# Performance work log

Hardware: AMD Instinct MI355X
Metric: run time of the kernel (lower is better)

Reference implementation:

```python
import jax, jax.numpy as jnp
import numpy as np

B, C, H, W = 8, 256, 64, 64
CM = C // 4          # mask channels (theta/phi out) = 64
CI = C - CM          # img channels = 192
EPS = 1e-5


def setup_inputs() -> dict:
    key = jax.random.key(0)
    ks = jax.random.split(key, 12)
    return {
        "x": jax.random.normal(ks[0], (B, C, H, W), dtype=jnp.float32),
        "g_w": jax.random.normal(ks[1], (C, C), dtype=jnp.float32) * 0.05,
        "g_b": jax.random.normal(ks[2], (C,), dtype=jnp.float32) * 0.01,
        "theta_w": jax.random.normal(ks[3], (CM, CM), dtype=jnp.float32) * 0.1,
        "theta_b": jax.random.normal(ks[4], (CM,), dtype=jnp.float32) * 0.01,
        "phi_w": jax.random.normal(ks[5], (CM, CI), dtype=jnp.float32) * 0.06,
        "phi_b": jax.random.normal(ks[6], (CM,), dtype=jnp.float32) * 0.01,
        "W_w": jax.random.normal(ks[7], (C, C), dtype=jnp.float32) * 0.05,
        "W_b": jax.random.normal(ks[8], (C,), dtype=jnp.float32) * 0.01,
        "bn_gamma": jax.random.normal(ks[9], (C,), dtype=jnp.float32) * 0.1 + 1.0,
        "bn_beta": jax.random.normal(ks[10], (C,), dtype=jnp.float32) * 0.01,
        "bn_mean": jax.random.normal(ks[11], (C,), dtype=jnp.float32) * 0.1,
        "bn_var": jnp.ones((C,), dtype=jnp.float32),
    }


def _conv1x1(t, w, b):
    # [B,Cin,H,W] x [Cout,Cin] -> [B,Cout,H,W]
    return jnp.einsum('bchw,oc->bohw', t, w) + b[None, :, None, None]


def _maxpool2(t):
    b, c, h, w = t.shape
    return t.reshape(b, c, h // 2, 2, w // 2, 2).max(axis=(3, 5))


def reference(x, g_w, g_b, theta_w, theta_b, phi_w, phi_b, W_w, W_b,
              bn_gamma, bn_beta, bn_mean, bn_var):
    b, c, h, w = x.shape
    ci = c // 4
    mask_ch = x[:, :ci]          # [B, C/4, H, W]
    img_ch = x[:, ci:]           # [B, 3C/4, H, W]

    # g: conv1x1 then 2x2 maxpool -> [B, C, N'] -> [B, N', C]
    g_x = _maxpool2(_conv1x1(x, g_w, g_b)).reshape(b, c, -1).transpose(0, 2, 1)
    # theta: conv1x1 on mask -> [B, N, C/4]
    theta_x = _conv1x1(mask_ch, theta_w, theta_b).reshape(b, ci, -1).transpose(0, 2, 1)
    # phi: conv1x1 on img then pool -> [B, C/4, N']
    phi_x = _maxpool2(_conv1x1(img_ch, phi_w, phi_b)).reshape(b, ci, -1)

    f = jnp.einsum('bnc,bcm->bnm', theta_x, phi_x)     # [B, N, N']
    f_div_C = jax.nn.softmax(f, axis=-1)
    y = jnp.einsum('bnm,bmc->bnc', f_div_C, g_x)       # [B, N, C]
    y = y.transpose(0, 2, 1).reshape(b, c, h, w)

    W_y = _conv1x1(y, W_w, W_b)
    # BatchNorm (inference form with running stats)
    inv = jax.lax.rsqrt(bn_var + EPS)
    W_y = (W_y - bn_mean[None, :, None, None]) * (inv * bn_gamma)[None, :, None, None] \
          + bn_beta[None, :, None, None]
    return W_y + x
```

## Files before the change

### kernel.cpp

```cpp
#include <hip/hip_runtime.h>
#include <hip/hip_bf16.h>

typedef __hip_bfloat16 bf16;
typedef unsigned short ushort;
typedef unsigned int uint;
typedef __attribute__((ext_vector_type(8))) short short8;
typedef __attribute__((ext_vector_type(4))) float f32x4;

#define Bn 8
#define Cn 256
#define Nn 4096
#define Mn 1024
#define EPSf 1e-5f

__device__ __forceinline__ float b2f(const bf16 v){ return __bfloat162float(v); }
__device__ __forceinline__ ushort f2bu(float f){
  uint u = __float_as_uint(f);
  return (ushort)((u + 0x7FFFu + ((u >> 16) & 1u)) >> 16);
}

__global__ __launch_bounds__(256) void transpose_kernel(
    const float* __restrict__ x, bf16* __restrict__ xT)
{
  __shared__ float xs[64][65];
  const int t = threadIdx.x;
  const int p0 = blockIdx.x*64, c0 = blockIdx.y*64, b = blockIdx.z;
  #pragma unroll
  for (int i = 0; i < 16; ++i) {
    int idx = t + i*256; int cl = idx >> 6, pl = idx & 63;
    xs[cl][pl] = x[((long)(b*Cn) + c0 + cl)*Nn + p0 + pl];
  }
  __syncthreads();
  ushort* xTu = (ushort*)xT;
  #pragma unroll
  for (int i = 0; i < 8; ++i) {
    int idx = t + i*256; int pl = idx >> 5, cp = idx & 31;
    uint u = (uint)f2bu(xs[cp*2][pl]) | ((uint)f2bu(xs[cp*2+1][pl]) << 16);
    *(uint*)(xTu + ((long)(b*Nn) + p0 + pl)*Cn + c0 + cp*2) = u;
  }
}

__global__ __launch_bounds__(256) void wcomb_kernel(
    const float* __restrict__ tw, const float* __restrict__ tb,
    const float* __restrict__ pw, const float* __restrict__ pb,
    const float* __restrict__ gw, const float* __restrict__ gb,
    bf16* __restrict__ Wcomb, float* __restrict__ bcomb)
{
  const int r = blockIdx.x, c = threadIdx.x;
  float v;
  if (r < 64)        v = (c < 64)  ? tw[r*64 + c]            : 0.f;
  else if (r < 128)  v = (c >= 64) ? pw[(r-64)*192 + (c-64)] : 0.f;
  else               v = gw[(r-128)*256 + c];
  Wcomb[r*256 + c] = __float2bfloat16(v);
  if (c == 0)
    bcomb[r] = (r < 64) ? tb[r] : (r < 128) ? pb[r-64] : gb[r-128];
}

__global__ __launch_bounds__(256) void gemm384_kernel(
    const bf16* __restrict__ xT, const bf16* __restrict__ Wcomb,
    const float* __restrict__ bcomb, bf16* __restrict__ Q,
    bf16* __restrict__ K, bf16* __restrict__ Vt)
{
  __shared__ union {
    struct { ushort As[128*40]; ushort Bs[128*40]; } g;
    float Pb[2][128][33];
  } sm;
  const int t = threadIdx.x;
  const int px = blockIdx.x, o0 = blockIdx.y*128, b = blockIdx.z;
  const int p0 = px*128;
  const int lane = t & 63, w = t >> 6;
  const int ql = lane & 15, quad = lane >> 4;
  const int wm = (w & 1)*64, wn = (w >> 1)*64;
  const ushort* xTu = (const ushort*)xT;
  const ushort* Wu  = (const ushort*)Wcomb;

  const int r0 = t >> 2, cq0 = t & 3;
  const int r1 = (t + 256) >> 2, cq1 = (t + 256) & 3;
  const ushort* aSrc0 = xTu + ((long)(b*Nn) + p0 + r0)*Cn + cq0*8;
  const ushort* aSrc1 = xTu + ((long)(b*Nn) + p0 + r1)*Cn + cq1*8;
  const ushort* bSrc0 = Wu + (o0 + r0)*Cn + cq0*8;
  const ushort* bSrc1 = Wu + (o0 + r1)*Cn + cq1*8;

  f32x4 acc[4][4];
  #pragma unroll
  for (int i = 0; i < 4; ++i)
    #pragma unroll
    for (int j = 0; j < 4; ++j) acc[i][j] = (f32x4){0.f,0.f,0.f,0.f};

  uint4 aReg0 = *(const uint4*)(aSrc0);
  uint4 aReg1 = *(const uint4*)(aSrc1);
  uint4 bReg0 = *(const uint4*)(bSrc0);
  uint4 bReg1 = *(const uint4*)(bSrc1);

  for (int kc = 0; kc < 8; ++kc) {
    __syncthreads();
    *(uint4*)(sm.g.As + r0*40 + cq0*8) = aReg0;
    *(uint4*)(sm.g.As + r1*40 + cq1*8) = aReg1;
    *(uint4*)(sm.g.Bs + r0*40 + cq0*8) = bReg0;
    *(uint4*)(sm.g.Bs + r1*40 + cq1*8) = bReg1;
    __syncthreads();
    if (kc < 7) {
      const int k1 = (kc + 1)*32;
      aReg0 = *(const uint4*)(aSrc0 + k1);
      aReg1 = *(const uint4*)(aSrc1 + k1);
      bReg0 = *(const uint4*)(bSrc0 + k1);
      bReg1 = *(const uint4*)(bSrc1 + k1);
    }
    short8 aF[4], bF[4];
    #pragma unroll
    for (int mi = 0; mi < 4; ++mi)
      aF[mi] = *(const short8*)(sm.g.As + (wm + mi*16 + ql)*40 + quad*8);
    #pragma unroll
    for (int ni = 0; ni < 4; ++ni)
      bF[ni] = *(const short8*)(sm.g.Bs + (wn + ni*16 + ql)*40 + quad*8);
    #pragma unroll
    for (int mi = 0; mi < 4; ++mi)
      #pragma unroll
      for (int ni = 0; ni < 4; ++ni)
        acc[mi][ni] = __builtin_amdgcn_mfma_f32_16x16x32_bf16(aF[mi], bF[ni], acc[mi][ni], 0, 0, 0);
  }
  float bias[4];
  #pragma unroll
  for (int ni = 0; ni < 4; ++ni) bias[ni] = bcomb[o0 + wn + ni*16 + ql];

  if (o0 == 0 && wn == 0) {
    #pragma unroll
    for (int mi = 0; mi < 4; ++mi)
      #pragma unroll
      for (int ni = 0; ni < 4; ++ni)
        #pragma unroll
        for (int r = 0; r < 4; ++r) {
          int p = p0 + wm + mi*16 + quad*4 + r;
          Q[((long)(b*Nn) + p)*64 + ni*16 + ql] = __float2bfloat16(acc[mi][ni][r] + bias[ni]);
        }
  }
  __syncthreads();
  if (o0 != 0 || wn == 64) {
    int g = w & 1;
    #pragma unroll
    for (int mi = 0; mi < 4; ++mi)
      #pragma unroll
      for (int ni = 0; ni < 4; ++ni) {
        float a0 = acc[mi][ni][0] + bias[ni], a1 = acc[mi][ni][1] + bias[ni];
        float a2 = acc[mi][ni][2] + bias[ni], a3 = acc[mi][ni][3] + bias[ni];
        int o = wn + ni*16 + ql;
        int wp = mi*8 + quad*2;
        sm.Pb[g][o][wp]     = fmaxf(a0, a1);
        sm.Pb[g][o][wp + 1] = fmaxf(a2, a3);
      }
  }
  __syncthreads();
  if (o0 == 0) {
    int wp = t & 31, og = t >> 5;
    ushort kv[8];
    #pragma unroll
    for (int j = 0; j < 8; ++j) {
      int o = 64 + og*8 + j;
      kv[j] = f2bu(fmaxf(sm.Pb[0][o][wp], sm.Pb[1][o][wp]));
    }
    *(uint4*)((ushort*)K + ((long)(b*Mn) + px*32 + wp)*64 + og*8) = *(uint4*)kv;
  } else {
    int ol = t >> 1, wp0 = (t & 1)*16;
    ushort vv[16];
    #pragma unroll
    for (int j = 0; j < 16; ++j)
      vv[j] = f2bu(fmaxf(sm.Pb[0][ol][wp0 + j], sm.Pb[1][ol][wp0 + j]));
    ushort* dst = (ushort*)Vt + ((long)(b*Cn) + (o0 - 128) + ol)*Mn + px*32 + wp0;
    *(uint4*)dst       = *(uint4*)(vv);
    *(uint4*)(dst + 8) = *(uint4*)(vv + 8);
  }
}

__global__ __launch_bounds__(512) void attn_kernel(
    const bf16* __restrict__ Q, const bf16* __restrict__ K, const bf16* __restrict__ Vt,
    bf16* __restrict__ Y)
{
  __shared__ __align__(16) ushort Ks[64*68];
  __shared__ __align__(16) ushort Vs[256*68];
  __shared__ __align__(16) ushort Ps[64*68];
  __shared__ float l_sh[2][64];

  const int t = threadIdx.x;
  const int b = blockIdx.y, q0 = blockIdx.x*64;
  const int lane = t & 63, w = t >> 6;
  const int ql = lane & 15, quad = lane >> 4;
  const int rt = w & 3;
  const int kh = w >> 2;
  const int rh = (w & 1)*32;
  const int cq = (w >> 1)*64;
  const ushort* Qu = (const ushort*)Q;
  const ushort* Ku = (const ushort*)K;
  const ushort* Vu = (const ushort*)Vt;

  const long qrow = (long)(b*Nn) + q0 + rt*16 + ql;
  short8 aQ0 = *(const short8*)(Qu + qrow*64 + quad*8);
  short8 aQ1 = *(const short8*)(Qu + qrow*64 + 32 + quad*8);

  const int ch = t & 7, rr = t >> 3;
  const ushort* kptr = Ku + ((long)(b*Mn) + rr)*64 + ch*8;
  const ushort* vptr0 = Vu + ((long)(b*Cn) + rr      )*Mn + ch*8;
  const ushort* vptr1 = Vu + ((long)(b*Cn) + rr +  64)*Mn + ch*8;
  const ushort* vptr2 = Vu + ((long)(b*Cn) + rr + 128)*Mn + ch*8;
  const ushort* vptr3 = Vu + ((long)(b*Cn) + rr + 192)*Mn + ch*8;

  float lrow[4];
  #pragma unroll
  for (int r = 0; r < 4; ++r) lrow[r] = 0.f;

  f32x4 acc[2][4];
  #pragma unroll
  for (int mi = 0; mi < 2; ++mi)
    #pragma unroll
    for (int ci = 0; ci < 4; ++ci) acc[mi][ci] = (f32x4){0.f,0.f,0.f,0.f};

  uint4 kreg = *(const uint4*)(kptr);
  uint4 vreg0 = *(const uint4*)(vptr0);
  uint4 vreg1 = *(const uint4*)(vptr1);
  uint4 vreg2 = *(const uint4*)(vptr2);
  uint4 vreg3 = *(const uint4*)(vptr3);

  for (int mt = 0; mt < 16; ++mt) {
    __syncthreads();
    *(uint4*)(Ks + rr*68 + ch*8) = kreg;
    *(uint4*)(Vs + (rr      )*68 + ch*8) = vreg0;
    *(uint4*)(Vs + (rr +  64)*68 + ch*8) = vreg1;
    *(uint4*)(Vs + (rr + 128)*68 + ch*8) = vreg2;
    *(uint4*)(Vs + (rr + 192)*68 + ch*8) = vreg3;
    __syncthreads();
    if (mt < 15) {
      const int m1 = (mt + 1)*64;
      kreg  = *(const uint4*)(kptr + (long)m1*64);
      vreg0 = *(const uint4*)(vptr0 + m1);
      vreg1 = *(const uint4*)(vptr1 + m1);
      vreg2 = *(const uint4*)(vptr2 + m1);
      vreg3 = *(const uint4*)(vptr3 + m1);
    }
    #pragma unroll
    for (int ct = 0; ct < 2; ++ct) {
      int kb = kh*32 + ct*16;
      short8 b0 = *(const short8*)(Ks + (kb + ql)*68 + quad*8);
      short8 b1 = *(const short8*)(Ks + (kb + ql)*68 + 32 + quad*8);
      f32x4 s = (f32x4){0.f,0.f,0.f,0.f};
      s = __builtin_amdgcn_mfma_f32_16x16x32_bf16(aQ0, b0, s, 0, 0, 0);
      s = __builtin_amdgcn_mfma_f32_16x16x32_bf16(aQ1, b1, s, 0, 0, 0);
      #pragma unroll
      for (int r = 0; r < 4; ++r) {
        float e = __expf(s[r]);
        lrow[r] += e;
        Ps[(rt*16 + quad*4 + r)*68 + kb + ql] = f2bu(e);
      }
    }
    __syncthreads();
    short8 aP0[2], aP1[2];
    #pragma unroll
    for (int mi = 0; mi < 2; ++mi) {
      aP0[mi] = *(const short8*)(Ps + (rh + mi*16 + ql)*68 + quad*8);
      aP1[mi] = *(const short8*)(Ps + (rh + mi*16 + ql)*68 + 32 + quad*8);
    }
    #pragma unroll
    for (int ci = 0; ci < 4; ++ci) {
      short8 b0 = *(const short8*)(Vs + (cq + ci*16 + ql)*68 + quad*8);
      short8 b1 = *(const short8*)(Vs + (cq + ci*16 + ql)*68 + 32 + quad*8);
      #pragma unroll
      for (int mi = 0; mi < 2; ++mi) {
        acc[mi][ci] = __builtin_amdgcn_mfma_f32_16x16x32_bf16(aP0[mi], b0, acc[mi][ci], 0, 0, 0);
        acc[mi][ci] = __builtin_amdgcn_mfma_f32_16x16x32_bf16(aP1[mi], b1, acc[mi][ci], 0, 0, 0);
      }
    }
  }
  #pragma unroll
  for (int r = 0; r < 4; ++r)
    #pragma unroll
    for (int off = 1; off < 16; off <<= 1)
      lrow[r] += __shfl_xor(lrow[r], off, 64);
  if (ql == 0) {
    #pragma unroll
    for (int r = 0; r < 4; ++r) l_sh[kh][rt*16 + quad*4 + r] = lrow[r];
  }
  __syncthreads();
  #pragma unroll
  for (int mi = 0; mi < 2; ++mi)
    #pragma unroll
    for (int r = 0; r < 4; ++r) {
      int row = rh + mi*16 + quad*4 + r;
      float inv = 1.f / (l_sh[0][row] + l_sh[1][row]);
      #pragma unroll
      for (int ci = 0; ci < 4; ++ci)
        Y[((long)(b*Nn) + q0 + row)*256 + cq + ci*16 + ql] = __float2bfloat16(acc[mi][ci][r]*inv);
    }
}

__global__ __launch_bounds__(256) void wconv_kernel(
    const bf16* __restrict__ Y, const float* __restrict__ Ww, const float* __restrict__ Wb,
    const float* __restrict__ gamma, const float* __restrict__ beta,
    const float* __restrict__ mean, const float* __restrict__ var,
    const float* __restrict__ x, float* __restrict__ out)
{
  __shared__ __align__(16) ushort As[128*40];
  __shared__ __align__(16) ushort Bs[128*40];
  __shared__ float ssc[128], ssh[128];
  const int t = threadIdx.x;
  const int n0 = blockIdx.x*128, o0 = blockIdx.y*128, b = blockIdx.z;
  const int lane = t & 63, w = t >> 6;
  const int ql = lane & 15, quad = lane >> 4;
  const int wm = (w & 1)*64, wn = (w >> 1)*64;
  const ushort* Yu = (const ushort*)Y;

  if (t < 128) {
    int o = o0 + t;
    float sc = gamma[o] * rsqrtf(var[o] + EPSf);
    ssc[t] = sc;
    ssh[t] = (Wb[o] - mean[o])*sc + beta[o];
  }

  const int ar[4] = { t >> 3, (t+256) >> 3, (t+512) >> 3, (t+768) >> 3 };
  const int ac[4] = { t & 7,  (t+256) & 7,  (t+512) & 7,  (t+768) & 7 };
  const int br0 = t >> 2, bc0 = t & 3;
  const int br1 = (t+256) >> 2, bc1 = (t+256) & 3;
  const float* aSrc[4] = {
    Ww + (o0 + ar[0])*Cn + ac[0]*4, Ww + (o0 + ar[1])*Cn + ac[1]*4,
    Ww + (o0 + ar[2])*Cn + ac[2]*4, Ww + (o0 + ar[3])*Cn + ac[3]*4 };
  const ushort* bSrc0 = Yu + ((long)(b*Nn) + n0 + br0)*Cn + bc0*8;
  const ushort* bSrc1 = Yu + ((long)(b*Nn) + n0 + br1)*Cn + bc1*8;

  f32x4 acc[4][4];
  #pragma unroll
  for (int i = 0; i < 4; ++i)
    #pragma unroll
    for (int j = 0; j < 4; ++j) acc[i][j] = (f32x4){0.f,0.f,0.f,0.f};

  float4 aReg[4];
  #pragma unroll
  for (int i = 0; i < 4; ++i) aReg[i] = *(const float4*)(aSrc[i]);
  uint4 bReg0 = *(const uint4*)(bSrc0);
  uint4 bReg1 = *(const uint4*)(bSrc1);

  for (int kc = 0; kc < 8; ++kc) {
    __syncthreads();
    #pragma unroll
    for (int i = 0; i < 4; ++i) {
      uint lo = (uint)f2bu(aReg[i].x) | ((uint)f2bu(aReg[i].y) << 16);
      uint hi = (uint)f2bu(aReg[i].z) | ((uint)f2bu(aReg[i].w) << 16);
      *(uint2*)(As + ar[i]*40 + ac[i]*4) = make_uint2(lo, hi);
    }
    *(uint4*)(Bs + br0*40 + bc0*8) = bReg0;
    *(uint4*)(Bs + br1*40 + bc1*8) = bReg1;
    __syncthreads();
    if (kc < 7) {
      const int k1 = (kc + 1)*32;
      #pragma unroll
      for (int i = 0; i < 4; ++i) aReg[i] = *(const float4*)(aSrc[i] + k1);
      bReg0 = *(const uint4*)(bSrc0 + k1);
      bReg1 = *(const uint4*)(bSrc1 + k1);
    }
    short8 aF[4], bF[4];
    #pragma unroll
    for (int mi = 0; mi < 4; ++mi)
      aF[mi] = *(const short8*)(As + (wm + mi*16 + ql)*40 + quad*8);
    #pragma unroll
    for (int ni = 0; ni < 4; ++ni)
      bF[ni] = *(const short8*)(Bs + (wn + ni*16 + ql)*40 + quad*8);
    #pragma unroll
    for (int mi = 0; mi < 4; ++mi)
      #pragma unroll
      for (int ni = 0; ni < 4; ++ni)
        acc[mi][ni] = __builtin_amdgcn_mfma_f32_16x16x32_bf16(aF[mi], bF[ni], acc[mi][ni], 0, 0, 0);
  }
  #pragma unroll
  for (int mi = 0; mi < 4; ++mi)
    #pragma unroll
    for (int r = 0; r < 4; ++r) {
      int ol = wm + mi*16 + quad*4 + r;
      int o = o0 + ol;
      float sc = ssc[ol], sh = ssh[ol];
      #pragma unroll
      for (int ni = 0; ni < 4; ++ni) {
        int n = n0 + wn + ni*16 + ql;
        long gidx = ((long)(b*Cn + o))*Nn + n;
        out[gidx] = acc[mi][ni][r]*sc + sh + x[gidx];
      }
    }
}

extern "C" void kernel_launch(void* const* d_in, const int* in_sizes, int n_in,
                              void* d_out, int out_size, void* d_ws, size_t ws_size,
                              hipStream_t stream)
{
  const float* x       = (const float*)d_in[0];
  const float* g_w     = (const float*)d_in[1];
  const float* g_b     = (const float*)d_in[2];
  const float* theta_w = (const float*)d_in[3];
  const float* theta_b = (const float*)d_in[4];
  const float* phi_w   = (const float*)d_in[5];
  const float* phi_b   = (const float*)d_in[6];
  const float* W_w     = (const float*)d_in[7];
  const float* W_b     = (const float*)d_in[8];
  const float* bn_g    = (const float*)d_in[9];
  const float* bn_b    = (const float*)d_in[10];
  const float* bn_m    = (const float*)d_in[11];
  const float* bn_v    = (const float*)d_in[12];
  float* out = (float*)d_out;

  bf16* wsb = (bf16*)d_ws;
  bf16* xT    = wsb;
  bf16* Y     = wsb;
  bf16* Q     = wsb + 8388608;
  bf16* K     = wsb + 10485760;
  bf16* Vt    = wsb + 11010048;
  bf16* Wcomb = wsb + 13107200;
  float* bcomb = (float*)(wsb + 13205504);

  transpose_kernel<<<dim3(64, 4, Bn), 256, 0, stream>>>(x, xT);
  wcomb_kernel<<<dim3(384), 256, 0, stream>>>(theta_w, theta_b, phi_w, phi_b, g_w, g_b, Wcomb, bcomb);
  gemm384_kernel<<<dim3(32, 3, Bn), 256, 0, stream>>>(xT, Wcomb, bcomb, Q, K, Vt);
  attn_kernel<<<dim3(64, Bn), 512, 0, stream>>>(Q, K, Vt, Y);
  wconv_kernel<<<dim3(32, 2, Bn), 256, 0, stream>>>(Y, W_w, W_b, bn_g, bn_b, bn_m, bn_v, x, out);
}
```

Measured before the change: 182.7 us.

## Pre-swizzle K/V into MFMA fragment layout and load directly to registers

The projection kernel now writes K and Vt in a layout that matches the MFMA B-operand fragments, so the attention kernel loads K and V straight from global memory into registers instead of staging them through shared memory. The attention loop is software-pipelined with a double-buffered P tile, which cuts barriers from three per tile to one and overlaps QK/exp of the next tile with PV of the previous one. In exchange, each wave loads its own V fragments, so some global/L2 traffic is duplicated across waves, and register pressure rises.

```diff
diff --git a/kernel.cpp b/kernel.cpp
--- a/kernel.cpp
+++ b/kernel.cpp
@@ -18,6 +18,7 @@
   uint u = __float_as_uint(f);
   return (ushort)((u + 0x7FFFu + ((u >> 16) & 1u)) >> 16);
 }
+
 
 __global__ __launch_bounds__(256) void transpose_kernel(
     const float* __restrict__ x, bf16* __restrict__ xT)
@@ -158,16 +159,20 @@
       int o = 64 + og*8 + j;
       kv[j] = f2bu(fmaxf(sm.Pb[0][o][wp], sm.Pb[1][o][wp]));
     }
-    *(uint4*)((ushort*)K + ((long)(b*Mn) + px*32 + wp)*64 + og*8) = *(uint4*)kv;
+    long kidx = ((long)(b*64) + px*2 + (wp>>4))*1024 + (og>>2)*512
+              + ((og&3)*16 + (wp&15))*8;
+    *(uint4*)((ushort*)K + kidx) = *(uint4*)kv;
   } else {
     int ol = t >> 1, wp0 = (t & 1)*16;
     ushort vv[16];
     #pragma unroll
     for (int j = 0; j < 16; ++j)
       vv[j] = f2bu(fmaxf(sm.Pb[0][ol][wp0 + j], sm.Pb[1][ol][wp0 + j]));
-    ushort* dst = (ushort*)Vt + ((long)(b*Cn) + (o0 - 128) + ol)*Mn + px*32 + wp0;
-    *(uint4*)dst       = *(uint4*)(vv);
-    *(uint4*)(dst + 8) = *(uint4*)(vv + 8);
+    int n = (o0 - 128) + ol;
+    long vbase = (long)(b)*262144 + (px>>1)*16384 + (n>>4)*1024 + (px&1)*512;
+    ushort* dst0 = (ushort*)Vt + vbase + ((wp0>>3)*16 + (n&15))*8;
+    *(uint4*)dst0         = *(uint4*)(vv);
+    *(uint4*)(dst0 + 128) = *(uint4*)(vv + 8);
   }
 }
 
@@ -175,9 +180,7 @@
     const bf16* __restrict__ Q, const bf16* __restrict__ K, const bf16* __restrict__ Vt,
     bf16* __restrict__ Y)
 {
-  __shared__ __align__(16) ushort Ks[64*68];
-  __shared__ __align__(16) ushort Vs[256*68];
-  __shared__ __align__(16) ushort Ps[64*68];
+  __shared__ __align__(16) ushort Ps[2][64*68];
   __shared__ float l_sh[2][64];
 
   const int t = threadIdx.x;
@@ -196,12 +199,8 @@
   short8 aQ0 = *(const short8*)(Qu + qrow*64 + quad*8);
   short8 aQ1 = *(const short8*)(Qu + qrow*64 + 32 + quad*8);
 
-  const int ch = t & 7, rr = t >> 3;
-  const ushort* kptr = Ku + ((long)(b*Mn) + rr)*64 + ch*8;
-  const ushort* vptr0 = Vu + ((long)(b*Cn) + rr      )*Mn + ch*8;
-  const ushort* vptr1 = Vu + ((long)(b*Cn) + rr +  64)*Mn + ch*8;
-  const ushort* vptr2 = Vu + ((long)(b*Cn) + rr + 128)*Mn + ch*8;
-  const ushort* vptr3 = Vu + ((long)(b*Cn) + rr + 192)*Mn + ch*8;
+  const ushort* kfp = Ku + ((long)(b*64) + kh*2)*1024 + lane*8;
+  const ushort* vfp = Vu + (long)(b)*262144 + (cq>>4)*1024 + lane*8;
 
   float lrow[4];
   #pragma unroll
@@ -213,61 +212,67 @@
     #pragma unroll
     for (int ci = 0; ci < 4; ++ci) acc[mi][ci] = (f32x4){0.f,0.f,0.f,0.f};
 
-  uint4 kreg = *(const uint4*)(kptr);
-  uint4 vreg0 = *(const uint4*)(vptr0);
-  uint4 vreg1 = *(const uint4*)(vptr1);
-  uint4 vreg2 = *(const uint4*)(vptr2);
-  uint4 vreg3 = *(const uint4*)(vptr3);
-
-  for (int mt = 0; mt < 16; ++mt) {
-    __syncthreads();
-    *(uint4*)(Ks + rr*68 + ch*8) = kreg;
-    *(uint4*)(Vs + (rr      )*68 + ch*8) = vreg0;
-    *(uint4*)(Vs + (rr +  64)*68 + ch*8) = vreg1;
-    *(uint4*)(Vs + (rr + 128)*68 + ch*8) = vreg2;
-    *(uint4*)(Vs + (rr + 192)*68 + ch*8) = vreg3;
-    __syncthreads();
-    if (mt < 15) {
-      const int m1 = (mt + 1)*64;
-      kreg  = *(const uint4*)(kptr + (long)m1*64);
-      vreg0 = *(const uint4*)(vptr0 + m1);
-      vreg1 = *(const uint4*)(vptr1 + m1);
-      vreg2 = *(const uint4*)(vptr2 + m1);
-      vreg3 = *(const uint4*)(vptr3 + m1);
-    }
+  short8 kf[4], vf[8];
+  auto LD_K = [&](int mt){
+    #pragma unroll
+    for (int ct = 0; ct < 2; ++ct)
+      #pragma unroll
+      for (int hf = 0; hf < 2; ++hf)
+        kf[ct*2+hf] = *(const short8*)(kfp + mt*4096 + ct*1024 + hf*512);
+  };
+  auto LD_V = [&](int mt){
+    #pragma unroll
+    for (int ci = 0; ci < 4; ++ci)
+      #pragma unroll
+      for (int hf = 0; hf < 2; ++hf)
+        vf[ci*2+hf] = *(const short8*)(vfp + mt*16384 + ci*1024 + hf*512);
+  };
+  auto QK = [&](int sel){
     #pragma unroll
     for (int ct = 0; ct < 2; ++ct) {
       int kb = kh*32 + ct*16;
-      short8 b0 = *(const short8*)(Ks + (kb + ql)*68 + quad*8);
-      short8 b1 = *(const short8*)(Ks + (kb + ql)*68 + 32 + quad*8);
       f32x4 s = (f32x4){0.f,0.f,0.f,0.f};
-      s = __builtin_amdgcn_mfma_f32_16x16x32_bf16(aQ0, b0, s, 0, 0, 0);
-      s = __builtin_amdgcn_mfma_f32_16x16x32_bf16(aQ1, b1, s, 0, 0, 0);
+      s = __builtin_amdgcn_mfma_f32_16x16x32_bf16(aQ0, kf[ct*2],   s, 0, 0, 0);
+      s = __builtin_amdgcn_mfma_f32_16x16x32_bf16(aQ1, kf[ct*2+1], s, 0, 0, 0);
       #pragma unroll
       for (int r = 0; r < 4; ++r) {
         float e = __expf(s[r]);
         lrow[r] += e;
-        Ps[(rt*16 + quad*4 + r)*68 + kb + ql] = f2bu(e);
+        Ps[sel][(rt*16 + quad*4 + r)*68 + kb + ql] = f2bu(e);
       }
     }
+  };
+  auto PV = [&](int sel){
+    short8 aP0[2], aP1[2];
+    #pragma unroll
+    for (int mi = 0; mi < 2; ++mi) {
+      aP0[mi] = *(const short8*)(&Ps[sel][(rh + mi*16 + ql)*68 + quad*8]);
+      aP1[mi] = *(const short8*)(&Ps[sel][(rh + mi*16 + ql)*68 + 32 + quad*8]);
+    }
+    #pragma unroll
+    for (int ci = 0; ci < 4; ++ci)
+      #pragma unroll
+      for (int mi = 0; mi < 2; ++mi) {
+        acc[mi][ci] = __builtin_amdgcn_mfma_f32_16x16x32_bf16(aP0[mi], vf[ci*2],   acc[mi][ci], 0, 0, 0);
+        acc[mi][ci] = __builtin_amdgcn_mfma_f32_16x16x32_bf16(aP1[mi], vf[ci*2+1], acc[mi][ci], 0, 0, 0);
+      }
+  };
+
+  LD_K(0);
+  LD_V(0);
+  QK(0);
+  LD_K(1);
+  __syncthreads();
+
+  for (int mt = 1; mt < 16; ++mt) {
+    PV((mt-1)&1);
+    LD_V(mt);
+    QK(mt&1);
+    LD_K((mt+1)&15);
     __syncthreads();
-    short8 aP0[2], aP1[2];
-    #pragma unroll
-    for (int mi = 0; mi < 2; ++mi) {
-      aP0[mi] = *(const short8*)(Ps + (rh + mi*16 + ql)*68 + quad*8);
-      aP1[mi] = *(const short8*)(Ps + (rh + mi*16 + ql)*68 + 32 + quad*8);
-    }
-    #pragma unroll
-    for (int ci = 0; ci < 4; ++ci) {
-      short8 b0 = *(const short8*)(Vs + (cq + ci*16 + ql)*68 + quad*8);
-      short8 b1 = *(const short8*)(Vs + (cq + ci*16 + ql)*68 + 32 + quad*8);
-      #pragma unroll
-      for (int mi = 0; mi < 2; ++mi) {
-        acc[mi][ci] = __builtin_amdgcn_mfma_f32_16x16x32_bf16(aP0[mi], b0, acc[mi][ci], 0, 0, 0);
-        acc[mi][ci] = __builtin_amdgcn_mfma_f32_16x16x32_bf16(aP1[mi], b1, acc[mi][ci], 0, 0, 0);
-      }
-    }
-  }
+  }
+  PV(1);
+
   #pragma unroll
   for (int r = 0; r < 4; ++r)
     #pragma unroll
```

Measured after the change: 174.7 us. 1.05x faster.
